# Kernel optimization log

Measured on AMD Instinct MI355X. Metric: run time of the kernel, lower is better.

The kernel has to match this reference:

```python
import jax, jax.numpy as jnp
import numpy as np

N_WORDS = 8192   # total words across all concepts
L = 24           # chars per word (padded)
D = 256          # word_vec_d
H = 8            # attention heads
DFF = 1024
VOCAB = 128
N_CONCEPTS = 1024
MAXW = 16        # max_words
GROUPS = 4       # n_names: 4 equal groups of concepts


def setup_inputs() -> dict:
    key = jax.random.key(0)
    ks = jax.random.split(key, 9)
    rng = np.random.default_rng(0)
    # char tokens in [1, VOCAB), ragged word lengths in [4, L], tail = 0 (pad)
    vals = rng.integers(1, VOCAB, size=(N_WORDS, L))
    lens = rng.integers(4, L + 1, size=(N_WORDS,))
    inputs = np.where(np.arange(L)[None, :] < lens[:, None], vals, 0)
    # ragged words-per-concept: alternate 4 / 12 -> sums to N_WORDS, <= MAXW
    counts = np.where(np.arange(N_CONCEPTS) % 2 == 0, 4, 12)
    concept_id = np.repeat(np.arange(N_CONCEPTS), counts)
    word_pos = np.concatenate([np.arange(c) for c in counts])

    def w(k, shape):
        return 0.02 * jax.random.normal(k, shape, jnp.float32)

    return {
        "inputs": jnp.asarray(inputs, jnp.int32),
        "concept_id": jnp.asarray(concept_id, jnp.int32),
        "word_pos": jnp.asarray(word_pos, jnp.int32),
        "n_concepts": N_CONCEPTS,
        "n_names": GROUPS,
        "we_emb": w(ks[0], (VOCAB, D)),
        "we_qkv": w(ks[1], (D, 3 * D)),
        "we_o": w(ks[2], (D, D)),
        "we_ff1": w(ks[3], (D, DFF)),
        "we_ff2": w(ks[4], (DFF, D)),
        "ne_qkv": w(ks[5], (D, 3 * D)),
        "ne_o": w(ks[6], (D, D)),
        "ne_ff1": w(ks[7], (D, DFF)),
        "ne_ff2": w(ks[8], (DFF, D)),
    }


def _ln(x):
    m = x.mean(-1, keepdims=True)
    v = ((x - m) ** 2).mean(-1, keepdims=True)
    return (x - m) * jax.lax.rsqrt(v + 1e-5)


def _mha(x, wqkv, wo, key_pad=None):
    n, l, d = x.shape
    hd = d // H
    q, k, v = jnp.split(x @ wqkv, 3, axis=-1)
    q = q.reshape(n, l, H, hd)
    k = k.reshape(n, l, H, hd)
    v = v.reshape(n, l, H, hd)
    s = jnp.einsum('nqhd,nkhd->nhqk', q, k) / jnp.sqrt(jnp.asarray(hd, x.dtype))
    if key_pad is not None:
        s = jnp.where(key_pad[:, None, None, :], -1e9, s)
    a = jax.nn.softmax(s, axis=-1)
    o = jnp.einsum('nhqk,nkhd->nqhd', a, v).reshape(n, l, d)
    return o @ wo


def _block(x, wqkv, wo, w1, w2, key_pad=None):
    h = _ln(x + _mha(x, wqkv, wo, key_pad))
    return _ln(h + jax.nn.relu(h @ w1) @ w2)


def reference(inputs, concept_id, word_pos, n_concepts, n_names,
              we_emb, we_qkv, we_o, we_ff1, we_ff2,
              ne_qkv, ne_o, ne_ff1, ne_ff2):
    pad_mask = inputs == 0  # [N_WORDS, L]
    x = we_emb[inputs]      # [N_WORDS, L, D]
    word_ft = _block(x, we_qkv, we_o, we_ff1, we_ff2, pad_mask)
    # masked mean over chars -> one vector per word
    np_mask = (~pad_mask)[..., None].astype(word_ft.dtype)  # [N_WORDS, L, 1]
    name_vec = (word_ft * np_mask).sum(1) / np_mask.sum(1)   # [N_WORDS, D]
    # ragged -> padded: one scatter instead of per-sample torch.cat
    padded = jnp.zeros((n_concepts, MAXW, name_vec.shape[-1]), name_vec.dtype)
    padded = padded.at[concept_id, word_pos].set(name_vec)   # [n_concepts, MAXW, D]
    name_ft = _block(padded, ne_qkv, ne_o, ne_ff1, ne_ff2)
    row_pad = (padded == 0).all(-1, keepdims=True)           # all-zero rows = pad words
    name_ft = jnp.where(row_pad, jnp.zeros((), name_ft.dtype), name_ft)
    counts = (name_ft != 0).sum(1).astype(name_ft.dtype)     # [n_concepts, D]
    pooled = name_ft.sum(1) / counts                         # [n_concepts, D]
    return tuple(jnp.split(pooled, n_names, axis=0))
```

## Files before the change

### kernel.cpp

```cpp
#include <hip/hip_runtime.h>
#include <hip/hip_bf16.h>

#define NWORDS 8192
#define LW 24
#define DIM 256
#define NHEAD 8
#define DFF 1024
#define NCONC 1024
#define MAXW 16
#define TN (NCONC * MAXW)

typedef float floatx4 __attribute__((ext_vector_type(4)));
typedef short shortx8 __attribute__((ext_vector_type(8)));

__device__ __forceinline__ float bf2f(ushort u) {
  union { uint u; float f; } v; v.u = ((uint)u) << 16; return v.f;
}
__device__ __forceinline__ ushort f2bf(float f) {
  union { float f; uint u; } v; v.f = f;
  return (ushort)((v.u + 0x7FFFu + ((v.u >> 16) & 1u)) >> 16);
}

__device__ __forceinline__ void load_lds16(const ushort* gsrc, ushort* lds) {
  __builtin_amdgcn_global_load_lds((const __attribute__((address_space(1))) void*)gsrc,
                                   (__attribute__((address_space(3))) void*)lds, 16, 0, 0);
}

#define STAGE_COL(lane) ((((lane) & 3) ^ (((lane) >> 3) & 3)) * 8)
#define FRAG_OFF(row, quad) (((row) * 32) + ((((quad) ^ (((row) >> 1) & 3))) * 8))

__global__ __launch_bounds__(256) void wprep(const float* __restrict__ W,
                                             ushort* __restrict__ WT, int K, int N) {
  int idx = blockIdx.x * 256 + threadIdx.x;
  if (idx < K * N) {
    int k = idx / N, n = idx % N;
    WT[n * K + k] = f2bf(W[idx]);
  }
}

__global__ __launch_bounds__(256) void embed4(const int* __restrict__ inputs,
                                              const float* __restrict__ we_emb,
                                              ushort* __restrict__ x, int ntok) {
  int idx = blockIdx.x * 256 + threadIdx.x;
  int t = idx >> 6, d = (idx & 63) * 4;
  if (t < ntok) {
    const float4 f = *(const float4*)&we_emb[inputs[t] * DIM + d];
    uint2 o;
    o.x = (uint)f2bf(f.x) | ((uint)f2bf(f.y) << 16);
    o.y = (uint)f2bf(f.z) | ((uint)f2bf(f.w) << 16);
    *(uint2*)&x[(size_t)t * DIM + d] = o;
  }
}

template <bool RELU>
__global__ __launch_bounds__(256) void gemm128(const ushort* __restrict__ A,
                                               const ushort* __restrict__ BT,
                                               ushort* __restrict__ C,
                                               int lda, int ldb, int ldc, int K) {
  __shared__ ushort As[2][128 * 32];
  __shared__ ushort Bs[2][128 * 32];
  const int tid = threadIdx.x;
  const int w = tid >> 6, lane = tid & 63;
  const int quad = lane >> 4, l16 = lane & 15;
  const long m0 = (long)blockIdx.y * 128;
  const long n0 = (long)blockIdx.x * 128;
  const int srow = lane >> 2;
  const int scol = STAGE_COL(lane);
  const int wr = (w >> 1) * 64, wc = (w & 1) * 64;

  floatx4 acc[4][4] = {};
  for (int k0 = 0; k0 < K; k0 += 64) {
#pragma unroll
    for (int s = 0; s < 2; s++)
#pragma unroll
      for (int i = 0; i < 2; i++) {
        int r = w * 32 + i * 16;
        load_lds16(&A[(m0 + r + srow) * lda + k0 + s * 32 + scol], &As[s][r * 32]);
        load_lds16(&BT[(n0 + r + srow) * ldb + k0 + s * 32 + scol], &Bs[s][r * 32]);
      }
    __syncthreads();
#pragma unroll
    for (int s = 0; s < 2; s++) {
      shortx8 a[4], b[4];
#pragma unroll
      for (int i = 0; i < 4; i++) a[i] = *(const shortx8*)&As[s][FRAG_OFF(wr + i * 16 + l16, quad)];
#pragma unroll
      for (int j = 0; j < 4; j++) b[j] = *(const shortx8*)&Bs[s][FRAG_OFF(wc + j * 16 + l16, quad)];
#pragma unroll
      for (int i = 0; i < 4; i++)
#pragma unroll
        for (int j = 0; j < 4; j++)
          acc[i][j] = __builtin_amdgcn_mfma_f32_16x16x32_bf16(a[i], b[j], acc[i][j], 0, 0, 0);
    }
    __syncthreads();
  }
#pragma unroll
  for (int i = 0; i < 4; i++)
#pragma unroll
    for (int j = 0; j < 4; j++)
#pragma unroll
      for (int r = 0; r < 4; r++) {
        float v = acc[i][j][r];
        if (RELU) v = fmaxf(v, 0.f);
        long m = m0 + wr + i * 16 + quad * 4 + r;
        long n = n0 + wc + j * 16 + l16;
        C[m * ldc + n] = f2bf(v);
      }
}

__global__ __launch_bounds__(256) void gemm_ln64(const ushort* __restrict__ A, int lda,
                                                 const ushort* __restrict__ BT,
                                                 const ushort* __restrict__ RES,
                                                 ushort* __restrict__ C,
                                                 int K) {
  __shared__ ushort As[2][64 * 32];
  __shared__ ushort Bs[2][256 * 32];
  __shared__ float red1[64 * 4];
  __shared__ float red2[64 * 4];
  const int tid = threadIdx.x;
  const int w = tid >> 6, lane = tid & 63;
  const int quad = lane >> 4, l16 = lane & 15;
  const long m0 = (long)blockIdx.x * 64;
  const int srow = lane >> 2;
  const int scol = STAGE_COL(lane);
  const int wc = w * 64;

  floatx4 acc[4][4] = {};
  for (int k0 = 0; k0 < K; k0 += 64) {
#pragma unroll
    for (int s = 0; s < 2; s++) {
      load_lds16(&A[(m0 + w * 16 + srow) * lda + k0 + s * 32 + scol], &As[s][(w * 16) * 32]);
#pragma unroll
      for (int i = 0; i < 4; i++) {
        int r = w * 64 + i * 16;
        load_lds16(&BT[(long)(r + srow) * K + k0 + s * 32 + scol], &Bs[s][r * 32]);
      }
    }
    __syncthreads();
#pragma unroll
    for (int s = 0; s < 2; s++) {
      shortx8 a[4], b[4];
#pragma unroll
      for (int i = 0; i < 4; i++) a[i] = *(const shortx8*)&As[s][FRAG_OFF(i * 16 + l16, quad)];
#pragma unroll
      for (int j = 0; j < 4; j++) b[j] = *(const shortx8*)&Bs[s][FRAG_OFF(wc + j * 16 + l16, quad)];
#pragma unroll
      for (int i = 0; i < 4; i++)
#pragma unroll
        for (int j = 0; j < 4; j++)
          acc[i][j] = __builtin_amdgcn_mfma_f32_16x16x32_bf16(a[i], b[j], acc[i][j], 0, 0, 0);
    }
    __syncthreads();
  }
#pragma unroll
  for (int i = 0; i < 4; i++)
#pragma unroll
    for (int r = 0; r < 4; r++) {
      int row = i * 16 + quad * 4 + r;
      float s1 = 0.f, s2 = 0.f;
#pragma unroll
      for (int j = 0; j < 4; j++) {
        float v = acc[i][j][r] + bf2f(RES[(m0 + row) * 256 + wc + j * 16 + l16]);
        acc[i][j][r] = v;
        s1 += v;
        s2 += v * v;
      }
#pragma unroll
      for (int off = 1; off < 16; off <<= 1) {
        s1 += __shfl_xor(s1, off);
        s2 += __shfl_xor(s2, off);
      }
      if (l16 == 0) { red1[row * 4 + w] = s1; red2[row * 4 + w] = s2; }
    }
  __syncthreads();
#pragma unroll
  for (int i = 0; i < 4; i++)
#pragma unroll
    for (int r = 0; r < 4; r++) {
      int row = i * 16 + quad * 4 + r;
      float s1 = red1[row * 4] + red1[row * 4 + 1] + red1[row * 4 + 2] + red1[row * 4 + 3];
      float s2 = red2[row * 4] + red2[row * 4 + 1] + red2[row * 4 + 2] + red2[row * 4 + 3];
      float mean = s1 * (1.f / 256.f);
      float rstd = rsqrtf(s2 * (1.f / 256.f) - mean * mean + 1e-5f);
#pragma unroll
      for (int j = 0; j < 4; j++)
        C[(m0 + row) * 256 + wc + j * 16 + l16] = f2bf((acc[i][j][r] - mean) * rstd);
    }
}

__global__ __launch_bounds__(256, 2) void ffn_fused(const ushort* __restrict__ H,
                                                    const ushort* __restrict__ W1T,
                                                    const ushort* __restrict__ W2T,
                                                    ushort* __restrict__ C,
                                                    int M) {
  __shared__ __align__(16) ushort As[8 * 48 * 32];
  __shared__ __align__(16) ushort Ss[8 * 48 * 32];
  __shared__ __align__(16) ushort Wb[256 * 32];
  const int tid = threadIdx.x;
  const int w = tid >> 6, lane = tid & 63;
  const int quad = lane >> 4, l16 = lane & 15;
  const long m0 = (long)blockIdx.x * 48;
  const int srow = lane >> 2;
  const int scol = STAGE_COL(lane);

#pragma unroll
  for (int t = 0; t < 6; t++) {
    int p = 2 * w + t / 3, ii = t % 3;
    load_lds16(&H[(m0 + ii * 16 + srow) * 256 + p * 32 + scol], &As[(p * 48 + ii * 16) * 32]);
  }

  floatx4 acc2[3][4] = {};
  for (int m = 0; m < 4; m++) {
    floatx4 acc1[4][3] = {};
    for (int p = 0; p < 8; p++) {
#pragma unroll
      for (int ii = 0; ii < 4; ii++)
        load_lds16(&W1T[(long)(m * 256 + w * 64 + ii * 16 + srow) * 256 + p * 32 + scol],
                   &Wb[(w * 64 + ii * 16) * 32]);
      __syncthreads();
      shortx8 a[4], b[3];
#pragma unroll
      for (int i = 0; i < 4; i++) a[i] = *(const shortx8*)&Wb[FRAG_OFF(w * 64 + i * 16 + l16, quad)];
#pragma unroll
      for (int j = 0; j < 3; j++)
        b[j] = *(const shortx8*)&As[p * 1536 + FRAG_OFF(j * 16 + l16, quad)];
#pragma unroll
      for (int i = 0; i < 4; i++)
#pragma unroll
        for (int j = 0; j < 3; j++)
          acc1[i][j] = __builtin_amdgcn_mfma_f32_16x16x32_bf16(a[i], b[j], acc1[i][j], 0, 0, 0);
      __syncthreads();
    }
#pragma unroll
    for (int i = 0; i < 4; i++) {
      int fb = w * 64 + i * 16 + quad * 4;
      int pf = fb >> 5, c = (fb >> 3) & 3, off = fb & 7;
#pragma unroll
      for (int j = 0; j < 3; j++) {
        int tok = j * 16 + l16;
        ushort4 pk;
        pk.x = f2bf(fmaxf(acc1[i][j][0], 0.f));
        pk.y = f2bf(fmaxf(acc1[i][j][1], 0.f));
        pk.z = f2bf(fmaxf(acc1[i][j][2], 0.f));
        pk.w = f2bf(fmaxf(acc1[i][j][3], 0.f));
        *(ushort4*)&Ss[(pf * 48 + tok) * 32 + ((c ^ ((tok >> 1) & 3)) << 3) + off] = pk;
      }
    }
    for (int p = 0; p < 8; p++) {
#pragma unroll
      for (int ii = 0; ii < 4; ii++)
        load_lds16(&W2T[(long)(w * 64 + ii * 16 + srow) * 1024 + m * 256 + p * 32 + scol],
                   &Wb[(w * 64 + ii * 16) * 32]);
      __syncthreads();
      shortx8 a[3], b[4];
#pragma unroll
      for (int i = 0; i < 3; i++)
        a[i] = *(const shortx8*)&Ss[p * 1536 + FRAG_OFF(i * 16 + l16, quad)];
#pragma unroll
      for (int j = 0; j < 4; j++) b[j] = *(const shortx8*)&Wb[FRAG_OFF(w * 64 + j * 16 + l16, quad)];
#pragma unroll
      for (int i = 0; i < 3; i++)
#pragma unroll
        for (int j = 0; j < 4; j++)
          acc2[i][j] = __builtin_amdgcn_mfma_f32_16x16x32_bf16(a[i], b[j], acc2[i][j], 0, 0, 0);
      __syncthreads();
    }
  }

  float* red1 = (float*)Ss;
  float* red2 = red1 + 192;
  const int wc = w * 64;
#pragma unroll
  for (int i = 0; i < 3; i++)
#pragma unroll
    for (int r = 0; r < 4; r++) {
      int row = i * 16 + quad * 4 + r;
      float s1 = 0.f, s2 = 0.f;
#pragma unroll
      for (int j = 0; j < 4; j++) {
        float v = acc2[i][j][r] + bf2f(H[(m0 + row) * 256 + wc + j * 16 + l16]);
        acc2[i][j][r] = v;
        s1 += v;
        s2 += v * v;
      }
#pragma unroll
      for (int off = 1; off < 16; off <<= 1) {
        s1 += __shfl_xor(s1, off);
        s2 += __shfl_xor(s2, off);
      }
      if (l16 == 0) { red1[row * 4 + w] = s1; red2[row * 4 + w] = s2; }
    }
  __syncthreads();
#pragma unroll
  for (int i = 0; i < 3; i++)
#pragma unroll
    for (int r = 0; r < 4; r++) {
      int row = i * 16 + quad * 4 + r;
      float s1 = red1[row * 4] + red1[row * 4 + 1] + red1[row * 4 + 2] + red1[row * 4 + 3];
      float s2 = red2[row * 4] + red2[row * 4 + 1] + red2[row * 4 + 2] + red2[row * 4 + 3];
      float mean = s1 * (1.f / 256.f);
      float rstd = rsqrtf(s2 * (1.f / 256.f) - mean * mean + 1e-5f);
      if (m0 + row < M) {
#pragma unroll
        for (int j = 0; j < 4; j++)
          C[(m0 + row) * 256 + wc + j * 16 + l16] = f2bf((acc2[i][j][r] - mean) * rstd);
      }
    }
}

template <int LSEQ, bool MASKED>
__global__ __launch_bounds__(256) void attn(const int* __restrict__ inputs,
                                            ushort* __restrict__ qkv) {
  __shared__ ushort Qs[LSEQ * 256];
  __shared__ ushort Ks[LSEQ * 256];
  __shared__ ushort Vs[LSEQ * 256];
  __shared__ float pads[LSEQ];
  const int blk = blockIdx.x;
  const int tid = threadIdx.x;
  ushort* base = qkv + (size_t)blk * LSEQ * 768;
  const uint4* src = (const uint4*)base;
  for (int i = tid; i < LSEQ * 96; i += 256) {
    int c = i / 96, part = i % 96;
    uint4 val = src[c * 96 + part];
    int sect = part >> 5, off = part & 31;
    ushort* dst = (sect == 0) ? Qs : (sect == 1 ? Ks : Vs);
    *(uint4*)&dst[c * 256 + off * 8] = val;
  }
  if (MASKED) {
    if (tid < LSEQ) pads[tid] = (inputs[blk * LSEQ + tid] == 0) ? 1.f : 0.f;
  }
  __syncthreads();
  if (tid < LSEQ * NHEAD) {
    const int i = tid % LSEQ, hh = tid / LSEQ;
    const int hb = hh * 32;
    float q[32];
    {
      const uint4* qr = (const uint4*)&Qs[i * 256 + hb];
#pragma unroll
      for (int u = 0; u < 4; u++) {
        uint4 ch = qr[u];
        const ushort* us = (const ushort*)&ch;
#pragma unroll
        for (int d = 0; d < 8; d++) q[u * 8 + d] = bf2f(us[d]);
      }
    }
    float s[LSEQ];
    float mx = -3e38f;
#pragma unroll
    for (int j = 0; j < LSEQ; j++) {
      const uint4* kr = (const uint4*)&Ks[j * 256 + hb];
      float a = 0.f;
#pragma unroll
      for (int u = 0; u < 4; u++) {
        uint4 ch = kr[u];
        const ushort* us = (const ushort*)&ch;
#pragma unroll
        for (int d = 0; d < 8; d++) a += q[u * 8 + d] * bf2f(us[d]);
      }
      a *= 0.17677669529663687f;
      if (MASKED && pads[j] != 0.f) a = -1e9f;
      s[j] = a;
      mx = fmaxf(mx, a);
    }
    float den = 0.f;
#pragma unroll
    for (int j = 0; j < LSEQ; j++) { s[j] = __expf(s[j] - mx); den += s[j]; }
    float inv = 1.f / den;
    float o[32] = {};
#pragma unroll
    for (int j = 0; j < LSEQ; j++) {
      float a = s[j] * inv;
      const uint4* vr = (const uint4*)&Vs[j * 256 + hb];
#pragma unroll
      for (int u = 0; u < 4; u++) {
        uint4 ch = vr[u];
        const ushort* us = (const ushort*)&ch;
#pragma unroll
        for (int d = 0; d < 8; d++) o[u * 8 + d] += a * bf2f(us[d]);
      }
    }
    ushort* orow = base + (size_t)i * 768 + hb;
#pragma unroll
    for (int d = 0; d < 32; d++) orow[d] = f2bf(o[d]);
  }
}

__global__ __launch_bounds__(256) void pool_scatter(const ushort* __restrict__ ft,
                                                    const int* __restrict__ inputs,
                                                    const int* __restrict__ cid,
                                                    const int* __restrict__ wpos,
                                                    ushort* __restrict__ padded,
                                                    int* __restrict__ flags) {
  int w = blockIdx.x, d = threadIdx.x;
  float s = 0.f;
  int cnt = 0;
  for (int c = 0; c < LW; c++) {
    if (inputs[w * LW + c] != 0) {
      s += bf2f(ft[((size_t)w * LW + c) * DIM + d]);
      cnt++;
    }
  }
  int slot = cid[w] * MAXW + wpos[w];
  padded[(size_t)slot * DIM + d] = f2bf(s / (float)cnt);
  if (d == 0) flags[slot] = 1;
}

__global__ __launch_bounds__(256) void final_pool(const ushort* __restrict__ nft,
                                                  const int* __restrict__ flags,
                                                  float* __restrict__ out) {
  int n = blockIdx.x, d = threadIdx.x;
  float s = 0.f;
  int cnt = 0;
  for (int wd = 0; wd < MAXW; wd++) {
    if (flags[n * MAXW + wd]) {
      s += bf2f(nft[((size_t)n * MAXW + wd) * DIM + d]);
      cnt++;
    }
  }
  out[n * DIM + d] = s / (float)cnt;
}

extern "C" void kernel_launch(void* const* d_in, const int* in_sizes, int n_in,
                              void* d_out, int out_size, void* d_ws, size_t ws_size,
                              hipStream_t stream) {
  const int* inputs = (const int*)d_in[0];
  const int* cid = (const int*)d_in[1];
  const int* wpos = (const int*)d_in[2];
  const float* we_emb = (const float*)d_in[5];
  const float* we_qkv = (const float*)d_in[6];
  const float* we_o = (const float*)d_in[7];
  const float* we_ff1 = (const float*)d_in[8];
  const float* we_ff2 = (const float*)d_in[9];
  const float* ne_qkv = (const float*)d_in[10];
  const float* ne_o = (const float*)d_in[11];
  const float* ne_ff1 = (const float*)d_in[12];
  const float* ne_ff2 = (const float*)d_in[13];
  float* out = (float*)d_out;

  int chunks = 4;
  if (ws_size >= 515000000UL) chunks = 1;
  else if (ws_size >= 263258112UL) chunks = 2;
  const int wpc = NWORDS / chunks;
  const int tpc = wpc * LW;

  const size_t X = (size_t)tpc * DIM * 2;
  const size_t Q = (size_t)tpc * 768 * 2;

  char* base = (char*)d_ws;
  ushort* x = (ushort*)(base);
  ushort* qkv = (ushort*)(base + X);
  ushort* h = (ushort*)(base + X + Q);
  ushort* ft = qkv;
  size_t pend = X + Q + X;
  ushort* padded = (ushort*)(base + pend);
  int* flags = (int*)(base + pend + 8388608);
  ushort* wT = (ushort*)(base + pend + 8454144);
  ushort* nqkv = (ushort*)(base);
  ushort* nh = (ushort*)(base + 25165824);
  ushort* nft = (ushort*)(base + 33554432);

  ushort* wqkvT = wT;
  ushort* woT = wT + 196608;
  ushort* wff1T = wT + 262144;
  ushort* wff2T = wT + 524288;
  ushort* nqkvT = wT + 786432;
  ushort* neoT = wT + 983040;
  ushort* neff1T = wT + 1048576;
  ushort* neff2T = wT + 1310720;

  wprep<<<768, 256, 0, stream>>>(we_qkv, wqkvT, 256, 768);
  wprep<<<256, 256, 0, stream>>>(we_o, woT, 256, 256);
  wprep<<<1024, 256, 0, stream>>>(we_ff1, wff1T, 256, 1024);
  wprep<<<1024, 256, 0, stream>>>(we_ff2, wff2T, 1024, 256);
  wprep<<<768, 256, 0, stream>>>(ne_qkv, nqkvT, 256, 768);
  wprep<<<256, 256, 0, stream>>>(ne_o, neoT, 256, 256);
  wprep<<<1024, 256, 0, stream>>>(ne_ff1, neff1T, 256, 1024);
  wprep<<<1024, 256, 0, stream>>>(ne_ff2, neff2T, 1024, 256);

  (void)hipMemsetAsync(padded, 0, (size_t)TN * DIM * 2, stream);
  (void)hipMemsetAsync(flags, 0, TN * 4, stream);

  for (int c = 0; c < chunks; c++) {
    const int* in_c = inputs + (size_t)c * wpc * LW;
    const int* cid_c = cid + (size_t)c * wpc;
    const int* wpos_c = wpos + (size_t)c * wpc;

    embed4<<<tpc / 4, 256, 0, stream>>>(in_c, we_emb, x, tpc);
    gemm128<false><<<dim3(6, tpc / 128), 256, 0, stream>>>(x, wqkvT, qkv, 256, 256, 768, 256);
    attn<24, true><<<wpc, 256, 0, stream>>>(in_c, qkv);
    gemm_ln64<<<tpc / 64, 256, 0, stream>>>(qkv, 768, woT, x, h, 256);
    ffn_fused<<<(tpc + 47) / 48, 256, 0, stream>>>(h, wff1T, wff2T, ft, tpc);
    pool_scatter<<<wpc, 256, 0, stream>>>(ft, in_c, cid_c, wpos_c, padded, flags);
  }

  gemm128<false><<<dim3(6, TN / 128), 256, 0, stream>>>(padded, nqkvT, nqkv, 256, 256, 768, 256);
  attn<16, false><<<NCONC, 256, 0, stream>>>(nullptr, nqkv);
  gemm_ln64<<<TN / 64, 256, 0, stream>>>(nqkv, 768, neoT, padded, nh, 256);
  ffn_fused<<<(TN + 47) / 48, 256, 0, stream>>>(nh, neff1T, neff2T, nft, TN);
  final_pool<<<NCONC, 256, 0, stream>>>(nft, flags, out);
}
```

Baseline: 1.088 ms.

## Load weight fragments directly from global memory instead of staging through LDS

In gemm_ln64 and ffn_fused, the weight operand is now read straight from global memory into MFMA registers, so the LDS staging buffers for weights are gone. This removes most per-k-step __syncthreads barriers and frees LDS, which lets ffn_fused raise its launch bound to 3 blocks per CU. In exchange, each wave issues uncoalesced 16-byte global loads for weights, relying on L2/L1 hits, and the loads are no longer shared across waves.

```diff
diff --git a/kernel.cpp b/kernel.cpp
--- a/kernel.cpp
+++ b/kernel.cpp
@@ -114,7 +114,6 @@
                                                  ushort* __restrict__ C,
                                                  int K) {
   __shared__ ushort As[2][64 * 32];
-  __shared__ ushort Bs[2][256 * 32];
   __shared__ float red1[64 * 4];
   __shared__ float red2[64 * 4];
   const int tid = threadIdx.x;
@@ -128,22 +127,17 @@
   floatx4 acc[4][4] = {};
   for (int k0 = 0; k0 < K; k0 += 64) {
 #pragma unroll
-    for (int s = 0; s < 2; s++) {
+    for (int s = 0; s < 2; s++)
       load_lds16(&A[(m0 + w * 16 + srow) * lda + k0 + s * 32 + scol], &As[s][(w * 16) * 32]);
-#pragma unroll
-      for (int i = 0; i < 4; i++) {
-        int r = w * 64 + i * 16;
-        load_lds16(&BT[(long)(r + srow) * K + k0 + s * 32 + scol], &Bs[s][r * 32]);
-      }
-    }
     __syncthreads();
 #pragma unroll
     for (int s = 0; s < 2; s++) {
       shortx8 a[4], b[4];
 #pragma unroll
+      for (int j = 0; j < 4; j++)
+        b[j] = *(const shortx8*)&BT[(long)(wc + j * 16 + l16) * K + k0 + s * 32 + quad * 8];
+#pragma unroll
       for (int i = 0; i < 4; i++) a[i] = *(const shortx8*)&As[s][FRAG_OFF(i * 16 + l16, quad)];
-#pragma unroll
-      for (int j = 0; j < 4; j++) b[j] = *(const shortx8*)&Bs[s][FRAG_OFF(wc + j * 16 + l16, quad)];
 #pragma unroll
       for (int i = 0; i < 4; i++)
 #pragma unroll
@@ -188,14 +182,13 @@
     }
 }
 
-__global__ __launch_bounds__(256, 2) void ffn_fused(const ushort* __restrict__ H,
+__global__ __launch_bounds__(256, 3) void ffn_fused(const ushort* __restrict__ H,
                                                     const ushort* __restrict__ W1T,
                                                     const ushort* __restrict__ W2T,
                                                     ushort* __restrict__ C,
                                                     int M) {
   __shared__ __align__(16) ushort As[8 * 48 * 32];
   __shared__ __align__(16) ushort Ss[8 * 48 * 32];
-  __shared__ __align__(16) ushort Wb[256 * 32];
   const int tid = threadIdx.x;
   const int w = tid >> 6, lane = tid & 63;
   const int quad = lane >> 4, l16 = lane & 15;
@@ -208,19 +201,18 @@
     int p = 2 * w + t / 3, ii = t % 3;
     load_lds16(&H[(m0 + ii * 16 + srow) * 256 + p * 32 + scol], &As[(p * 48 + ii * 16) * 32]);
   }
+  __syncthreads();
 
   floatx4 acc2[3][4] = {};
   for (int m = 0; m < 4; m++) {
     floatx4 acc1[4][3] = {};
+#pragma unroll 2
     for (int p = 0; p < 8; p++) {
-#pragma unroll
-      for (int ii = 0; ii < 4; ii++)
-        load_lds16(&W1T[(long)(m * 256 + w * 64 + ii * 16 + srow) * 256 + p * 32 + scol],
-                   &Wb[(w * 64 + ii * 16) * 32]);
-      __syncthreads();
       shortx8 a[4], b[3];
 #pragma unroll
-      for (int i = 0; i < 4; i++) a[i] = *(const shortx8*)&Wb[FRAG_OFF(w * 64 + i * 16 + l16, quad)];
+      for (int i = 0; i < 4; i++)
+        a[i] = *(const shortx8*)&W1T[(long)(m * 256 + w * 64 + i * 16 + l16) * 256 + p * 32 +
+                                     quad * 8];
 #pragma unroll
       for (int j = 0; j < 3; j++)
         b[j] = *(const shortx8*)&As[p * 1536 + FRAG_OFF(j * 16 + l16, quad)];
@@ -229,8 +221,8 @@
 #pragma unroll
         for (int j = 0; j < 3; j++)
           acc1[i][j] = __builtin_amdgcn_mfma_f32_16x16x32_bf16(a[i], b[j], acc1[i][j], 0, 0, 0);
-      __syncthreads();
-    }
+    }
+    __syncthreads();
 #pragma unroll
     for (int i = 0; i < 4; i++) {
       int fb = w * 64 + i * 16 + quad * 4;
@@ -246,26 +238,25 @@
         *(ushort4*)&Ss[(pf * 48 + tok) * 32 + ((c ^ ((tok >> 1) & 3)) << 3) + off] = pk;
       }
     }
+    __syncthreads();
+#pragma unroll 2
     for (int p = 0; p < 8; p++) {
-#pragma unroll
-      for (int ii = 0; ii < 4; ii++)
-        load_lds16(&W2T[(long)(w * 64 + ii * 16 + srow) * 1024 + m * 256 + p * 32 + scol],
-                   &Wb[(w * 64 + ii * 16) * 32]);
-      __syncthreads();
       shortx8 a[3], b[4];
+#pragma unroll
+      for (int j = 0; j < 4; j++)
+        b[j] = *(const shortx8*)&W2T[(long)(w * 64 + j * 16 + l16) * 1024 + m * 256 + p * 32 +
+                                     quad * 8];
 #pragma unroll
       for (int i = 0; i < 3; i++)
         a[i] = *(const shortx8*)&Ss[p * 1536 + FRAG_OFF(i * 16 + l16, quad)];
 #pragma unroll
-      for (int j = 0; j < 4; j++) b[j] = *(const shortx8*)&Wb[FRAG_OFF(w * 64 + j * 16 + l16, quad)];
-#pragma unroll
       for (int i = 0; i < 3; i++)
 #pragma unroll
         for (int j = 0; j < 4; j++)
           acc2[i][j] = __builtin_amdgcn_mfma_f32_16x16x32_bf16(a[i], b[j], acc2[i][j], 0, 0, 0);
-      __syncthreads();
-    }
-  }
+    }
+  }
+  __syncthreads();
 
   float* red1 = (float*)Ss;
   float* red2 = red1 + 192;
```

Measured after the change: 1.319 ms. 1.21x slower.

## Load FFN weight fragments directly from global into registers with double buffering

Applied to the files above, without the earlier changes.

The fused FFN kernel no longer stages W1/W2 tiles through a shared LDS buffer. Each wave now reads its own weight fragments straight from global memory into registers, using two register buffers that are prefetched one K-step ahead. This removes two block-wide barriers per K-step and frees LDS, so launch bounds are raised from 2 to 3 blocks per SM. The costs are uncoalesced 16-byte global reads that depend on L2 hit rates, and higher register pressure under the tighter occupancy target.

```diff
diff --git a/kernel.cpp b/kernel.cpp
--- a/kernel.cpp
+++ b/kernel.cpp
@@ -188,14 +188,13 @@
     }
 }
 
-__global__ __launch_bounds__(256, 2) void ffn_fused(const ushort* __restrict__ H,
+__global__ __launch_bounds__(256, 3) void ffn_fused(const ushort* __restrict__ H,
                                                     const ushort* __restrict__ W1T,
                                                     const ushort* __restrict__ W2T,
                                                     ushort* __restrict__ C,
                                                     int M) {
   __shared__ __align__(16) ushort As[8 * 48 * 32];
   __shared__ __align__(16) ushort Ss[8 * 48 * 32];
-  __shared__ __align__(16) ushort Wb[256 * 32];
   const int tid = threadIdx.x;
   const int w = tid >> 6, lane = tid & 63;
   const int quad = lane >> 4, l16 = lane & 15;
@@ -208,19 +207,20 @@
     int p = 2 * w + t / 3, ii = t % 3;
     load_lds16(&H[(m0 + ii * 16 + srow) * 256 + p * 32 + scol], &As[(p * 48 + ii * 16) * 32]);
   }
+  __syncthreads();
 
   floatx4 acc2[3][4] = {};
   for (int m = 0; m < 4; m++) {
     floatx4 acc1[4][3] = {};
-    for (int p = 0; p < 8; p++) {
-#pragma unroll
-      for (int ii = 0; ii < 4; ii++)
-        load_lds16(&W1T[(long)(m * 256 + w * 64 + ii * 16 + srow) * 256 + p * 32 + scol],
-                   &Wb[(w * 64 + ii * 16) * 32]);
-      __syncthreads();
-      shortx8 a[4], b[3];
-#pragma unroll
-      for (int i = 0; i < 4; i++) a[i] = *(const shortx8*)&Wb[FRAG_OFF(w * 64 + i * 16 + l16, quad)];
+    const ushort* w1b = W1T + ((long)(m * 256 + w * 64 + l16)) * 256 + quad * 8;
+    shortx8 c0[4], c1[4];
+#pragma unroll
+    for (int i = 0; i < 4; i++) c0[i] = *(const shortx8*)(w1b + i * 4096);
+#pragma unroll
+    for (int i = 0; i < 4; i++) c1[i] = *(const shortx8*)(w1b + i * 4096 + 32);
+#pragma unroll
+    for (int p = 0; p < 8; p += 2) {
+      shortx8 b[3];
 #pragma unroll
       for (int j = 0; j < 3; j++)
         b[j] = *(const shortx8*)&As[p * 1536 + FRAG_OFF(j * 16 + l16, quad)];
@@ -228,9 +228,25 @@
       for (int i = 0; i < 4; i++)
 #pragma unroll
         for (int j = 0; j < 3; j++)
-          acc1[i][j] = __builtin_amdgcn_mfma_f32_16x16x32_bf16(a[i], b[j], acc1[i][j], 0, 0, 0);
-      __syncthreads();
-    }
+          acc1[i][j] = __builtin_amdgcn_mfma_f32_16x16x32_bf16(c0[i], b[j], acc1[i][j], 0, 0, 0);
+      if (p + 2 < 8) {
+#pragma unroll
+        for (int i = 0; i < 4; i++) c0[i] = *(const shortx8*)(w1b + i * 4096 + (p + 2) * 32);
+      }
+#pragma unroll
+      for (int j = 0; j < 3; j++)
+        b[j] = *(const shortx8*)&As[(p + 1) * 1536 + FRAG_OFF(j * 16 + l16, quad)];
+#pragma unroll
+      for (int i = 0; i < 4; i++)
+#pragma unroll
+        for (int j = 0; j < 3; j++)
+          acc1[i][j] = __builtin_amdgcn_mfma_f32_16x16x32_bf16(c1[i], b[j], acc1[i][j], 0, 0, 0);
+      if (p + 3 < 8) {
+#pragma unroll
+        for (int i = 0; i < 4; i++) c1[i] = *(const shortx8*)(w1b + i * 4096 + (p + 3) * 32);
+      }
+    }
+    __syncthreads();
 #pragma unroll
     for (int i = 0; i < 4; i++) {
       int fb = w * 64 + i * 16 + quad * 4;
@@ -246,26 +262,45 @@
         *(ushort4*)&Ss[(pf * 48 + tok) * 32 + ((c ^ ((tok >> 1) & 3)) << 3) + off] = pk;
       }
     }
-    for (int p = 0; p < 8; p++) {
-#pragma unroll
-      for (int ii = 0; ii < 4; ii++)
-        load_lds16(&W2T[(long)(w * 64 + ii * 16 + srow) * 1024 + m * 256 + p * 32 + scol],
-                   &Wb[(w * 64 + ii * 16) * 32]);
-      __syncthreads();
-      shortx8 a[3], b[4];
+    __syncthreads();
+    const ushort* w2b = W2T + ((long)(w * 64 + l16)) * 1024 + m * 256 + quad * 8;
+    shortx8 d0[4], d1[4];
+#pragma unroll
+    for (int j = 0; j < 4; j++) d0[j] = *(const shortx8*)(w2b + (long)j * 16384);
+#pragma unroll
+    for (int j = 0; j < 4; j++) d1[j] = *(const shortx8*)(w2b + (long)j * 16384 + 32);
+#pragma unroll
+    for (int p = 0; p < 8; p += 2) {
+      shortx8 a[3];
 #pragma unroll
       for (int i = 0; i < 3; i++)
         a[i] = *(const shortx8*)&Ss[p * 1536 + FRAG_OFF(i * 16 + l16, quad)];
 #pragma unroll
-      for (int j = 0; j < 4; j++) b[j] = *(const shortx8*)&Wb[FRAG_OFF(w * 64 + j * 16 + l16, quad)];
-#pragma unroll
       for (int i = 0; i < 3; i++)
 #pragma unroll
         for (int j = 0; j < 4; j++)
-          acc2[i][j] = __builtin_amdgcn_mfma_f32_16x16x32_bf16(a[i], b[j], acc2[i][j], 0, 0, 0);
-      __syncthreads();
-    }
-  }
+          acc2[i][j] = __builtin_amdgcn_mfma_f32_16x16x32_bf16(a[i], d0[j], acc2[i][j], 0, 0, 0);
+      if (p + 2 < 8) {
+#pragma unroll
+        for (int j = 0; j < 4; j++)
+          d0[j] = *(const shortx8*)(w2b + (long)j * 16384 + (p + 2) * 32);
+      }
+#pragma unroll
+      for (int i = 0; i < 3; i++)
+        a[i] = *(const shortx8*)&Ss[(p + 1) * 1536 + FRAG_OFF(i * 16 + l16, quad)];
+#pragma unroll
+      for (int i = 0; i < 3; i++)
+#pragma unroll
+        for (int j = 0; j < 4; j++)
+          acc2[i][j] = __builtin_amdgcn_mfma_f32_16x16x32_bf16(a[i], d1[j], acc2[i][j], 0, 0, 0);
+      if (p + 3 < 8) {
+#pragma unroll
+        for (int j = 0; j < 4; j++)
+          d1[j] = *(const shortx8*)(w2b + (long)j * 16384 + (p + 3) * 32);
+      }
+    }
+  }
+  __syncthreads();
 
   float* red1 = (float*)Ss;
   float* red2 = red1 + 192;
```

New measurement: 1.247 ms. +14.6%, slower.

## Load FFN weight fragments directly from global into registers with double buffering

Applied to the files above, without the earlier changes.

In the fused FFN kernel, each wave now reads its own W1/W2 MFMA fragments straight from global memory into registers. It prefetches two k-steps ahead instead of staging the weights through a shared LDS buffer. This removes the Wb LDS array and the two __syncthreads per k-step, keeping barriers only around the Ss hand-off. The cost is more register pressure and non-coalesced 16-byte global reads that rely on L2 reuse of the weights across blocks.

```diff
diff --git a/kernel.cpp b/kernel.cpp
--- a/kernel.cpp
+++ b/kernel.cpp
@@ -195,7 +195,6 @@
                                                     int M) {
   __shared__ __align__(16) ushort As[8 * 48 * 32];
   __shared__ __align__(16) ushort Ss[8 * 48 * 32];
-  __shared__ __align__(16) ushort Wb[256 * 32];
   const int tid = threadIdx.x;
   const int w = tid >> 6, lane = tid & 63;
   const int quad = lane >> 4, l16 = lane & 15;
@@ -208,19 +207,20 @@
     int p = 2 * w + t / 3, ii = t % 3;
     load_lds16(&H[(m0 + ii * 16 + srow) * 256 + p * 32 + scol], &As[(p * 48 + ii * 16) * 32]);
   }
+  __syncthreads();
 
   floatx4 acc2[3][4] = {};
   for (int m = 0; m < 4; m++) {
     floatx4 acc1[4][3] = {};
+    const ushort* w1b = W1T + ((long)(m * 256 + w * 64 + l16)) * 256 + quad * 8;
+    shortx8 wb[2][4];
+#pragma unroll
+    for (int i = 0; i < 4; i++) wb[0][i] = *(const shortx8*)(w1b + i * 4096);
+#pragma unroll
+    for (int i = 0; i < 4; i++) wb[1][i] = *(const shortx8*)(w1b + i * 4096 + 32);
+#pragma unroll
     for (int p = 0; p < 8; p++) {
-#pragma unroll
-      for (int ii = 0; ii < 4; ii++)
-        load_lds16(&W1T[(long)(m * 256 + w * 64 + ii * 16 + srow) * 256 + p * 32 + scol],
-                   &Wb[(w * 64 + ii * 16) * 32]);
-      __syncthreads();
-      shortx8 a[4], b[3];
-#pragma unroll
-      for (int i = 0; i < 4; i++) a[i] = *(const shortx8*)&Wb[FRAG_OFF(w * 64 + i * 16 + l16, quad)];
+      shortx8 b[3];
 #pragma unroll
       for (int j = 0; j < 3; j++)
         b[j] = *(const shortx8*)&As[p * 1536 + FRAG_OFF(j * 16 + l16, quad)];
@@ -228,9 +228,15 @@
       for (int i = 0; i < 4; i++)
 #pragma unroll
         for (int j = 0; j < 3; j++)
-          acc1[i][j] = __builtin_amdgcn_mfma_f32_16x16x32_bf16(a[i], b[j], acc1[i][j], 0, 0, 0);
-      __syncthreads();
-    }
+          acc1[i][j] =
+              __builtin_amdgcn_mfma_f32_16x16x32_bf16(wb[p & 1][i], b[j], acc1[i][j], 0, 0, 0);
+      if (p + 2 < 8) {
+#pragma unroll
+        for (int i = 0; i < 4; i++)
+          wb[p & 1][i] = *(const shortx8*)(w1b + i * 4096 + (p + 2) * 32);
+      }
+    }
+    __syncthreads();
 #pragma unroll
     for (int i = 0; i < 4; i++) {
       int fb = w * 64 + i * 16 + quad * 4;
@@ -246,26 +252,33 @@
         *(ushort4*)&Ss[(pf * 48 + tok) * 32 + ((c ^ ((tok >> 1) & 3)) << 3) + off] = pk;
       }
     }
+    __syncthreads();
+    const ushort* w2b = W2T + ((long)(w * 64 + l16)) * 1024 + m * 256 + quad * 8;
+    shortx8 db[2][4];
+#pragma unroll
+    for (int j = 0; j < 4; j++) db[0][j] = *(const shortx8*)(w2b + (long)j * 16384);
+#pragma unroll
+    for (int j = 0; j < 4; j++) db[1][j] = *(const shortx8*)(w2b + (long)j * 16384 + 32);
+#pragma unroll
     for (int p = 0; p < 8; p++) {
-#pragma unroll
-      for (int ii = 0; ii < 4; ii++)
-        load_lds16(&W2T[(long)(w * 64 + ii * 16 + srow) * 1024 + m * 256 + p * 32 + scol],
-                   &Wb[(w * 64 + ii * 16) * 32]);
-      __syncthreads();
-      shortx8 a[3], b[4];
+      shortx8 a[3];
 #pragma unroll
       for (int i = 0; i < 3; i++)
         a[i] = *(const shortx8*)&Ss[p * 1536 + FRAG_OFF(i * 16 + l16, quad)];
 #pragma unroll
-      for (int j = 0; j < 4; j++) b[j] = *(const shortx8*)&Wb[FRAG_OFF(w * 64 + j * 16 + l16, quad)];
-#pragma unroll
       for (int i = 0; i < 3; i++)
 #pragma unroll
         for (int j = 0; j < 4; j++)
-          acc2[i][j] = __builtin_amdgcn_mfma_f32_16x16x32_bf16(a[i], b[j], acc2[i][j], 0, 0, 0);
-      __syncthreads();
-    }
-  }
+          acc2[i][j] =
+              __builtin_amdgcn_mfma_f32_16x16x32_bf16(a[i], db[p & 1][j], acc2[i][j], 0, 0, 0);
+      if (p + 2 < 8) {
+#pragma unroll
+        for (int j = 0; j < 4; j++)
+          db[p & 1][j] = *(const shortx8*)(w2b + (long)j * 16384 + (p + 2) * 32);
+      }
+    }
+  }
+  __syncthreads();
 
   float* red1 = (float*)Ss;
   float* red2 = red1 + 192;
```

After: 1.259 ms. +15.7%, slower.
